# Kernel optimization log

Measured on AMD Instinct MI355X. Metric: run time of the kernel, lower is better.

Reference implementation:

```python
import math
import jax, jax.numpy as jnp
import numpy as np

D_MODEL = 1024
NUM_HEADS = 16
D_K = D_MODEL // NUM_HEADS
RANK = 16
B, L = 2, 2048


def setup_inputs() -> dict:
    key = jax.random.key(0)
    ks = jax.random.split(key, 10)
    w_scale = 0.02  # keep activations well-scaled like trained linears
    return {
        "x_q": jax.random.normal(ks[0], (B, L, D_MODEL), jnp.float32),
        "x_kv": jax.random.normal(ks[1], (B, L, D_MODEL), jnp.float32),
        "Wq": jax.random.normal(ks[2], (D_MODEL, D_MODEL), jnp.float32) * w_scale,
        "bq": jnp.zeros((D_MODEL,), jnp.float32),
        "Wk": jax.random.normal(ks[3], (D_MODEL, D_MODEL), jnp.float32) * w_scale,
        "bk": jnp.zeros((D_MODEL,), jnp.float32),
        "Wv": jax.random.normal(ks[4], (D_MODEL, D_MODEL), jnp.float32) * w_scale,
        "bv": jnp.zeros((D_MODEL,), jnp.float32),
        "Wo": jax.random.normal(ks[5], (D_MODEL, D_MODEL), jnp.float32) * w_scale,
        "bo": jnp.zeros((D_MODEL,), jnp.float32),
        "U_bil": jax.random.normal(ks[6], (NUM_HEADS, D_K, RANK), jnp.float32) * 0.02,
        "V_bil": jax.random.normal(ks[7], (NUM_HEADS, D_K, RANK), jnp.float32) * 0.02,
        "padding_mask": jnp.zeros((B, L), bool),  # True = padded KV position
    }


def reference(x_q, x_kv, Wq, bq, Wk, bk, Wv, bv, Wo, bo, U_bil, V_bil, padding_mask):
    b, l, _ = x_q.shape
    # torch nn.Linear: y = x @ W.T + b
    Q = (x_q @ Wq.T + bq).reshape(b, l, NUM_HEADS, D_K).transpose(0, 2, 1, 3)  # [B,H,L,dk]
    K = (x_kv @ Wk.T + bk).reshape(b, l, NUM_HEADS, D_K).transpose(0, 2, 1, 3)
    V = (x_kv @ Wv.T + bv).reshape(b, l, NUM_HEADS, D_K).transpose(0, 2, 1, 3)
    # low-rank bilinear projections: [B,H,L,rank]
    Q_proj = jnp.einsum("bhld,hdr->bhlr", Q, U_bil)
    K_proj = jnp.einsum("bhld,hdr->bhlr", K, V_bil)
    scores = jnp.einsum("bhqr,bhkr->bhqk", Q_proj, K_proj) / math.sqrt(RANK)  # [B,H,L,L]
    scores = jnp.where(padding_mask[:, None, None, :], jnp.float32(-10000.0), scores)
    attn = jax.nn.softmax(scores, axis=-1)  # dropout is identity in eval mode
    ctx = jnp.einsum("bhqk,bhkd->bhqd", attn, V)
    ctx = ctx.transpose(0, 2, 1, 3).reshape(b, l, D_MODEL)
    return ctx @ Wo.T + bo
```

## Files before the change

### kernel.cpp

```cpp
#include <hip/hip_runtime.h>
#include <hip/hip_bf16.h>

#define DM   1024
#define NH   16
#define DK   64
#define RK   16
#define BB   2
#define LL   2048
#define TT   (BB*LL)
#define HRK  256


typedef float f4   __attribute__((ext_vector_type(4)));
typedef float f16v __attribute__((ext_vector_type(16)));
typedef short s8v  __attribute__((ext_vector_type(8)));

static __device__ __forceinline__ unsigned short f2b(float f) {
  __hip_bfloat16 h = __float2bfloat16(f);
  unsigned short u;
  __builtin_memcpy(&u, &h, 2);
  return u;
}
static __device__ __forceinline__ float b2f(unsigned short u) {
  __hip_bfloat16 h;
  __builtin_memcpy(&h, &u, 2);
  return __bfloat162float(h);
}

__global__ __launch_bounds__(256) void cast_all(
    const float* __restrict__ s0, unsigned short* __restrict__ d0, int n0,
    const float* __restrict__ s1, unsigned short* __restrict__ d1, int n1,
    const float* __restrict__ s2, unsigned short* __restrict__ d2, int n2,
    const float* __restrict__ s3, unsigned short* __restrict__ d3, int n3) {
  const float* s; unsigned short* d; int n;
  switch (blockIdx.y) {
    case 0:  s = s0; d = d0; n = n0; break;
    case 1:  s = s1; d = d1; n = n1; break;
    case 2:  s = s2; d = d2; n = n2; break;
    default: s = s3; d = d3; n = n3; break;
  }
  for (int i = blockIdx.x*256 + threadIdx.x; i < n; i += gridDim.x*256) {
    const float4 v = ((const float4*)s)[i];
    ushort4 o;
    o.x = f2b(v.x); o.y = f2b(v.y); o.z = f2b(v.z); o.w = f2b(v.w);
    ((ushort4*)d)[i] = o;
  }
}

__global__ __launch_bounds__(256) void fuse_w(
    const float* __restrict__ Wq, const float* __restrict__ Wk,
    const float* __restrict__ Uq, const float* __restrict__ Uk,
    unsigned short* __restrict__ Aq, unsigned short* __restrict__ Ak) {
  const float* W = blockIdx.z ? Wk : Wq;
  const float* U = blockIdx.z ? Uk : Uq;
  unsigned short* At = blockIdx.z ? Ak : Aq;
  __shared__ float Us[64][16];
  __shared__ float Ws[4][64];
  const int i0 = blockIdx.x * 64;
  const int h  = blockIdx.y;
  const int tid = threadIdx.x;
  const int il = tid & 63, rr = tid >> 6;
  for (int t = tid; t < 64*16; t += 256)
    Us[t >> 4][t & 15] = U[(size_t)(h*DK + (t >> 4))*RK + (t & 15)];
  float acc[4] = {};
  for (int d0 = 0; d0 < DK; d0 += 4) {
    __syncthreads();
    Ws[rr][il] = W[(size_t)(h*DK + d0 + rr)*DM + i0 + il];
    __syncthreads();
#pragma unroll
    for (int dd = 0; dd < 4; ++dd) {
      const float w = Ws[dd][il];
#pragma unroll
      for (int j = 0; j < 4; ++j)
        acc[j] += w * Us[d0 + dd][rr*4 + j];
    }
  }
#pragma unroll
  for (int j = 0; j < 4; ++j)
    At[(size_t)(h*RK + rr*4 + j)*DM + i0 + il] = f2b(acc[j]);
}

__global__ void bias2(const float* __restrict__ bq, const float* __restrict__ bk,
                      const float* __restrict__ Uq, const float* __restrict__ Uk,
                      float* __restrict__ bpq, float* __restrict__ bpk) {
  const int t = threadIdx.x;
  const float* b = (t < 256) ? bq : bk;
  const float* U = (t < 256) ? Uq : Uk;
  float* bp = (t < 256) ? bpq : bpk;
  const int hr = t & 255, h = hr >> 4, r = hr & 15;
  float acc = 0.f;
  for (int d = 0; d < DK; ++d)
    acc += b[h*DK + d] * U[(size_t)(h*DK + d)*RK + r];
  bp[hr] = acc;
}

__global__ __launch_bounds__(256) void vsum_k(
    const unsigned short* __restrict__ Vt, float* __restrict__ Vsum) {
  const int h = blockIdx.x, b = blockIdx.y;
  const int d = threadIdx.x >> 2, part = threadIdx.x & 3;
  const unsigned short* row = Vt + ((size_t)b*DM + h*DK + d)*LL + part*512;
  float s = 0.f;
  for (int i = 0; i < 512; i += 8) {
    const s8v v = *(const s8v*)&row[i];
#pragma unroll
    for (int j = 0; j < 8; ++j) s += b2f((unsigned short)v[j]);
  }
  s += __shfl_xor(s, 1);
  s += __shfl_xor(s, 2);
  if (part == 0) Vsum[((size_t)b*NH + h)*DK + d] = s;
}

template<int N_, int MODE, int AF32>
__global__ __launch_bounds__(256) void gemm64(
    const void* __restrict__ A0, const void* __restrict__ A1,
    const unsigned short* __restrict__ B0, const unsigned short* __restrict__ B1,
    const float* __restrict__ bi0, const float* __restrict__ bi1,
    void* __restrict__ C0, void* __restrict__ C1) {
  const void* Agv = blockIdx.z ? A1 : A0;
  const unsigned short* Bg = blockIdx.z ? B1 : B0;
  const float* bias = blockIdx.z ? bi1 : bi0;
  void* Cgv = blockIdx.z ? C1 : C0;
  __shared__ unsigned short Xs[64*40];
  __shared__ unsigned short Bs[128*40];
  const int t0 = blockIdx.x * 64, n0 = blockIdx.y * 128;
  const int tid = threadIdx.x, wave = tid >> 6, lane = tid & 63;
  const int quad = lane >> 4, l15 = lane & 15;
  const int nh = wave * 32;

  const f4 z = {0.f, 0.f, 0.f, 0.f};
  f4 acc[4][2];
#pragma unroll
  for (int a = 0; a < 4; ++a) { acc[a][0] = z; acc[a][1] = z; }

  for (int k0 = 0; k0 < DM; k0 += 32) {
    __syncthreads();
    {
      const int ar = tid >> 2, ap = tid & 3;
      if (AF32) {
        const float* Af = (const float*)Agv;
        const float4 x0 = *(const float4*)&Af[(size_t)(t0 + ar)*DM + k0 + ap*8];
        const float4 x1 = *(const float4*)&Af[(size_t)(t0 + ar)*DM + k0 + ap*8 + 4];
        s8v v;
        v[0]=(short)f2b(x0.x); v[1]=(short)f2b(x0.y);
        v[2]=(short)f2b(x0.z); v[3]=(short)f2b(x0.w);
        v[4]=(short)f2b(x1.x); v[5]=(short)f2b(x1.y);
        v[6]=(short)f2b(x1.z); v[7]=(short)f2b(x1.w);
        *(s8v*)&Xs[ar*40 + ap*8] = v;
      } else {
        *(s8v*)&Xs[ar*40 + ap*8] =
            *(const s8v*)&((const unsigned short*)Agv)[(size_t)(t0 + ar)*DM + k0 + ap*8];
      }
      const int br = tid >> 1, bp = tid & 1;
      *(s8v*)&Bs[br*40 + bp*16] =
          *(const s8v*)&Bg[(size_t)(n0 + br)*DM + k0 + bp*16];
      *(s8v*)&Bs[br*40 + bp*16 + 8] =
          *(const s8v*)&Bg[(size_t)(n0 + br)*DM + k0 + bp*16 + 8];
    }
    __syncthreads();

    s8v af[4], bf[2];
#pragma unroll
    for (int ms = 0; ms < 4; ++ms)
      af[ms] = *(const s8v*)&Xs[(ms*16 + l15)*40 + quad*8];
#pragma unroll
    for (int ns = 0; ns < 2; ++ns)
      bf[ns] = *(const s8v*)&Bs[(nh + ns*16 + l15)*40 + quad*8];
#pragma unroll
    for (int ms = 0; ms < 4; ++ms)
#pragma unroll
      for (int ns = 0; ns < 2; ++ns)
        acc[ms][ns] = __builtin_amdgcn_mfma_f32_16x16x32_bf16(
            af[ms], bf[ns], acc[ms][ns], 0, 0, 0);
  }

#pragma unroll
  for (int ms = 0; ms < 4; ++ms) {
    const int tb = t0 + ms*16 + quad*4;
#pragma unroll
    for (int ns = 0; ns < 2; ++ns) {
      const int o = n0 + nh + ns*16 + l15;
      const float bv = bias[o];
      f4 a = acc[ms][ns];
      if (MODE == 0) {
        float* C = (float*)Cgv;
#pragma unroll
        for (int rg = 0; rg < 4; ++rg)
          C[(size_t)(tb + rg)*N_ + o] = a[rg] + bv;
      } else if (MODE == 1) {
        unsigned short* C = (unsigned short*)Cgv;
#pragma unroll
        for (int rg = 0; rg < 4; ++rg)
          C[(size_t)(tb + rg)*N_ + o] = f2b(a[rg] + bv);
      } else {
        unsigned short* C = (unsigned short*)Cgv;
        const int bb = tb >> 11, l = tb & 2047;
        ushort4 pk;
        pk.x = f2b(a[0] + bv); pk.y = f2b(a[1] + bv);
        pk.z = f2b(a[2] + bv); pk.w = f2b(a[3] + bv);
        *(ushort4*)&C[((size_t)bb*DM + o)*LL + l] = pk;
      }
    }
  }
}

__global__ __launch_bounds__(256) void attention_v4(
    const unsigned short* __restrict__ Qp, const unsigned short* __restrict__ Kp,
    const unsigned short* __restrict__ Vt, const float* __restrict__ Vsum,
    const unsigned char* __restrict__ msk, float* __restrict__ ctx) {
  __shared__ unsigned short Ks[64*24];
  __shared__ unsigned short Vs[64*72];
  __shared__ unsigned short Es[4][32*48];
  __shared__ float denW[4][32];
  const int q0 = blockIdx.x * 128, h = blockIdx.y, b = blockIdx.z;
  const int tid = threadIdx.x, w = tid >> 6, lane = tid & 63;
  const int l31 = lane & 31, hi = lane >> 5;
  unsigned short* __restrict__ Ew = Es[w];

  const s8v qfrag = *(const s8v*)&Qp[
      (size_t)(b*LL + q0 + w*32 + l31)*HRK + h*RK + hi*8];

  f16v acc0, acc1, z16;
#pragma unroll
  for (int i = 0; i < 16; ++i) { acc0[i] = 0.f; acc1[i] = 0.f; z16[i] = 0.f; }
  float den = 0.f;

  for (int k0 = 0; k0 < LL; k0 += 64) {
    __syncthreads();
    if (tid < 128) {
      const int row = tid >> 1, part = tid & 1;
      *(s8v*)&Ks[row*24 + part*8] =
          *(const s8v*)&Kp[(size_t)(b*LL + k0 + row)*HRK + h*RK + part*8];
    }
    {
      const int d = tid >> 2, p = tid & 3;
      const size_t gv = ((size_t)b*DM + h*DK + d)*LL + k0 + p*16;
      *(s8v*)&Vs[d*72 + p*16]     = *(const s8v*)&Vt[gv];
      *(s8v*)&Vs[d*72 + p*16 + 8] = *(const s8v*)&Vt[gv + 8];
    }
    const unsigned long long mb =
        __ballot(msk[(size_t)b*LL + k0 + lane] != 0);
    __syncthreads();

#pragma unroll
    for (int nt = 0; nt < 2; ++nt) {
      const s8v kf = *(const s8v*)&Ks[(nt*32 + l31)*24 + hi*8];
      f16v s = __builtin_amdgcn_mfma_f32_32x32x16_bf16(kf, qfrag, z16, 0, 0, 0);
#pragma unroll
      for (int r = 0; r < 4; ++r) {
        ushort4 pk;
#pragma unroll
        for (int j = 0; j < 4; ++j) {
          const int kloc = nt*32 + j + 8*r + 4*hi;
          float em = __expf(s[r*4 + j] * 0.25f);
          if ((mb >> kloc) & 1ull) em = 0.f;
          den += em;
          ((unsigned short*)&pk)[j] = f2b(em - 1.f);
        }
        *(ushort4*)&Ew[l31*48 + nt*32 + r*8 + 4*hi] = pk;
      }
    }
#pragma unroll
    for (int kc = 0; kc < 4; ++kc) {
      const s8v ef  = *(const s8v*)&Ew[l31*48 + kc*16 + hi*8];
      const s8v vf0 = *(const s8v*)&Vs[l31*72 + kc*16 + hi*8];
      const s8v vf1 = *(const s8v*)&Vs[(32 + l31)*72 + kc*16 + hi*8];
      acc0 = __builtin_amdgcn_mfma_f32_32x32x16_bf16(ef, vf0, acc0, 0, 0, 0);
      acc1 = __builtin_amdgcn_mfma_f32_32x32x16_bf16(ef, vf1, acc1, 0, 0, 0);
    }
  }

  den += __shfl_xor(den, 32);
  if (hi == 0) denW[w][l31] = 1.f / fmaxf(den, 1e-30f);

  const float vs0 = Vsum[((size_t)b*NH + h)*DK + l31];
  const float vs1 = Vsum[((size_t)b*NH + h)*DK + 32 + l31];

#pragma unroll
  for (int rg = 0; rg < 16; ++rg) {
    const int qr = (rg & 3) + 8*(rg >> 2) + 4*hi;
    const float inv = denW[w][qr];
    const size_t row = (size_t)(b*LL + q0 + w*32 + qr)*DM + h*DK;
    ctx[row + l31]      = (vs0 + acc0[rg]) * inv;
    ctx[row + 32 + l31] = (vs1 + acc1[rg]) * inv;
  }
}

extern "C" void kernel_launch(void* const* d_in, const int* in_sizes, int n_in,
                              void* d_out, int out_size, void* d_ws, size_t ws_size,
                              hipStream_t stream) {
  (void)in_sizes; (void)n_in; (void)out_size; (void)ws_size;
  const float* x_q   = (const float*)d_in[0];
  const float* x_kv  = (const float*)d_in[1];
  const float* Wq    = (const float*)d_in[2];
  const float* bq    = (const float*)d_in[3];
  const float* Wk    = (const float*)d_in[4];
  const float* bk    = (const float*)d_in[5];
  const float* Wv    = (const float*)d_in[6];
  const float* bv    = (const float*)d_in[7];
  const float* Wo    = (const float*)d_in[8];
  const float* bo    = (const float*)d_in[9];
  const float* U_bil = (const float*)d_in[10];
  const float* V_bil = (const float*)d_in[11];
  const unsigned char* pmask = (const unsigned char*)d_in[12];
  float* out = (float*)d_out;

  char* w = (char*)d_ws;
  unsigned short* xq_b  = (unsigned short*)(w);
  unsigned short* xkv_b = (unsigned short*)(w +  8388608);
  unsigned short* Wv_b  = (unsigned short*)(w + 16777216);
  unsigned short* Wo_b  = (unsigned short*)(w + 18874368);
  unsigned short* Atq   = (unsigned short*)(w + 20971520);
  unsigned short* Atk   = (unsigned short*)(w + 21495808);
  float*          bpq   = (float*)(w + 22020096);
  float*          bpk   = (float*)(w + 22021120);
  unsigned short* Qp    = (unsigned short*)(w + 22022144);
  unsigned short* Kp    = (unsigned short*)(w + 24119296);
  unsigned short* Vt    = (unsigned short*)(w + 26216448);
  float*          Vsum  = (float*)(w + 34605056);
  float*          ctx   = (float*)w;

  cast_all<<<dim3(1024, 4), 256, 0, stream>>>(
      x_q, xq_b, TT*DM/4, x_kv, xkv_b, TT*DM/4,
      Wv, Wv_b, DM*DM/4,  Wo, Wo_b, DM*DM/4);
  fuse_w<<<dim3(DM/64, NH, 2), 256, 0, stream>>>(Wq, Wk, U_bil, V_bil, Atq, Atk);
  bias2<<<1, 512, 0, stream>>>(bq, bk, U_bil, V_bil, bpq, bpk);
  gemm64<HRK, 1, 0><<<dim3(64, 2, 2), 256, 0, stream>>>(
      xq_b, xkv_b, Atq, Atk, bpq, bpk, Qp, Kp);
  gemm64<DM, 2, 0><<<dim3(64, 8, 1), 256, 0, stream>>>(
      xkv_b, xkv_b, Wv_b, Wv_b, bv, bv, Vt, Vt);
  vsum_k<<<dim3(NH, BB), 256, 0, stream>>>(Vt, Vsum);
  attention_v4<<<dim3(LL/128, NH, BB), 256, 0, stream>>>(
      Qp, Kp, Vt, Vsum, pmask, ctx);
  gemm64<DM, 0, 1><<<dim3(64, 8, 1), 256, 0, stream>>>(
      ctx, ctx, Wo_b, Wo_b, bo, bo, out, out);
}
```

Baseline: 274.6 us.

## Double-buffer K/V tiles with register prefetch and keep softmax probabilities in registers

Rewrites the attention kernel to double-buffer the K and V tiles in shared memory, prefetching the next tile into registers so global loads overlap compute. One barrier per iteration replaces two. Probabilities are packed with v_cvt_pk_bf16_f32 and rearranged into MFMA operand layout with cross-half lane shuffles instead of a round trip through shared memory. A fast path also skips per-element masking when a tile has no padded keys. These changes add register pressure and shuffle work in exchange for less LDS traffic and fewer synchronisations.

New measurement: 276.7 us. Within noise of the previous version (+0.8%).

```diff
diff --git a/kernel.cpp b/kernel.cpp
--- a/kernel.cpp
+++ b/kernel.cpp
@@ -14,6 +14,8 @@
 typedef float f4   __attribute__((ext_vector_type(4)));
 typedef float f16v __attribute__((ext_vector_type(16)));
 typedef short s8v  __attribute__((ext_vector_type(8)));
+typedef unsigned int u2v __attribute__((ext_vector_type(2)));
+typedef unsigned int u4v __attribute__((ext_vector_type(4)));
 
 static __device__ __forceinline__ unsigned short f2b(float f) {
   __hip_bfloat16 h = __float2bfloat16(f);
@@ -203,70 +205,127 @@
   }
 }
 
-__global__ __launch_bounds__(256) void attention_v4(
+template<bool MASKED>
+static __device__ __forceinline__ void softmax_pack(
+    const f16v& s0, const f16v& s1, const unsigned long long mb, const int hi,
+    float& den, unsigned int (&Pd)[2][4][2]) {
+#pragma unroll
+  for (int nt = 0; nt < 2; ++nt) {
+    const f16v& sv = nt ? s1 : s0;
+#pragma unroll
+    for (int r = 0; r < 4; ++r) {
+      float ep[4];
+#pragma unroll
+      for (int j = 0; j < 4; ++j) {
+        float em = __expf(sv[r*4 + j] * 0.25f);
+        if (MASKED) {
+          const int kloc = nt*32 + j + 8*r + 4*hi;
+          if ((mb >> kloc) & 1ull) em = 0.f;
+        }
+        den += em;
+        ep[j] = em - 1.f;
+      }
+      asm("v_cvt_pk_bf16_f32 %0, %1, %2"
+          : "=v"(Pd[nt][r][0]) : "v"(ep[0]), "v"(ep[1]));
+      asm("v_cvt_pk_bf16_f32 %0, %1, %2"
+          : "=v"(Pd[nt][r][1]) : "v"(ep[2]), "v"(ep[3]));
+    }
+  }
+}
+
+__global__ __launch_bounds__(256) void attention_v5(
     const unsigned short* __restrict__ Qp, const unsigned short* __restrict__ Kp,
     const unsigned short* __restrict__ Vt, const float* __restrict__ Vsum,
     const unsigned char* __restrict__ msk, float* __restrict__ ctx) {
-  __shared__ unsigned short Ks[64*24];
-  __shared__ unsigned short Vs[64*72];
-  __shared__ unsigned short Es[4][32*48];
+  __shared__ __align__(16) unsigned short Ks[2][2][64][8];
+  __shared__ __align__(16) unsigned short Vs[2][8][64][8];
   __shared__ float denW[4][32];
   const int q0 = blockIdx.x * 128, h = blockIdx.y, b = blockIdx.z;
   const int tid = threadIdx.x, w = tid >> 6, lane = tid & 63;
   const int l31 = lane & 31, hi = lane >> 5;
-  unsigned short* __restrict__ Ew = Es[w];
 
   const s8v qfrag = *(const s8v*)&Qp[
       (size_t)(b*LL + q0 + w*32 + l31)*HRK + h*RK + hi*8];
 
+  const int sr = tid >> 2, sp = tid & 3;
+  const unsigned short* __restrict__ Vrow =
+      Vt + ((size_t)b*DM + h*DK + sr)*LL;
+  const unsigned short* __restrict__ Kbase =
+      Kp + ((size_t)b*LL + sr)*HRK + h*RK + sp*4;
+  const unsigned char*  __restrict__ Mrow = msk + (size_t)b*LL + lane;
+
+  u2v kpre; s8v vpre0, vpre1;
+  unsigned char mcur, mnext;
+
+  kpre  = *(const u2v*)&Kbase[0];
+  vpre0 = *(const s8v*)&Vrow[sp*16];
+  vpre1 = *(const s8v*)&Vrow[sp*16 + 8];
+  mcur  = Mrow[0];
+  *(u2v*)&Ks[0][sp>>1][sr][(sp&1)*4] = kpre;
+  *(s8v*)&Vs[0][sp*2][sr][0]   = vpre0;
+  *(s8v*)&Vs[0][sp*2+1][sr][0] = vpre1;
+  kpre  = *(const u2v*)&Kbase[(size_t)64*HRK];
+  vpre0 = *(const s8v*)&Vrow[64 + sp*16];
+  vpre1 = *(const s8v*)&Vrow[64 + sp*16 + 8];
+  mnext = Mrow[64];
+  __syncthreads();
+
   f16v acc0, acc1, z16;
 #pragma unroll
   for (int i = 0; i < 16; ++i) { acc0[i] = 0.f; acc1[i] = 0.f; z16[i] = 0.f; }
   float den = 0.f;
 
-  for (int k0 = 0; k0 < LL; k0 += 64) {
-    __syncthreads();
-    if (tid < 128) {
-      const int row = tid >> 1, part = tid & 1;
-      *(s8v*)&Ks[row*24 + part*8] =
-          *(const s8v*)&Kp[(size_t)(b*LL + k0 + row)*HRK + h*RK + part*8];
-    }
-    {
-      const int d = tid >> 2, p = tid & 3;
-      const size_t gv = ((size_t)b*DM + h*DK + d)*LL + k0 + p*16;
-      *(s8v*)&Vs[d*72 + p*16]     = *(const s8v*)&Vt[gv];
-      *(s8v*)&Vs[d*72 + p*16 + 8] = *(const s8v*)&Vt[gv + 8];
-    }
-    const unsigned long long mb =
-        __ballot(msk[(size_t)b*LL + k0 + lane] != 0);
-    __syncthreads();
-
-#pragma unroll
-    for (int nt = 0; nt < 2; ++nt) {
-      const s8v kf = *(const s8v*)&Ks[(nt*32 + l31)*24 + hi*8];
-      f16v s = __builtin_amdgcn_mfma_f32_32x32x16_bf16(kf, qfrag, z16, 0, 0, 0);
-#pragma unroll
-      for (int r = 0; r < 4; ++r) {
-        ushort4 pk;
-#pragma unroll
-        for (int j = 0; j < 4; ++j) {
-          const int kloc = nt*32 + j + 8*r + 4*hi;
-          float em = __expf(s[r*4 + j] * 0.25f);
-          if ((mb >> kloc) & 1ull) em = 0.f;
-          den += em;
-          ((unsigned short*)&pk)[j] = f2b(em - 1.f);
-        }
-        *(ushort4*)&Ew[l31*48 + nt*32 + r*8 + 4*hi] = pk;
-      }
-    }
+  for (int t = 0; t < LL/64; ++t) {
+    const int cur = t & 1;
+    const unsigned long long mb = __ballot(mcur != 0);
+
+    const s8v kf0 = *(const s8v*)&Ks[cur][hi][l31][0];
+    const s8v kf1 = *(const s8v*)&Ks[cur][hi][32 + l31][0];
+    s8v vf[4][2];
 #pragma unroll
     for (int kc = 0; kc < 4; ++kc) {
-      const s8v ef  = *(const s8v*)&Ew[l31*48 + kc*16 + hi*8];
-      const s8v vf0 = *(const s8v*)&Vs[l31*72 + kc*16 + hi*8];
-      const s8v vf1 = *(const s8v*)&Vs[(32 + l31)*72 + kc*16 + hi*8];
-      acc0 = __builtin_amdgcn_mfma_f32_32x32x16_bf16(ef, vf0, acc0, 0, 0, 0);
-      acc1 = __builtin_amdgcn_mfma_f32_32x32x16_bf16(ef, vf1, acc1, 0, 0, 0);
-    }
+      vf[kc][0] = *(const s8v*)&Vs[cur][kc*2 + hi][l31][0];
+      vf[kc][1] = *(const s8v*)&Vs[cur][kc*2 + hi][32 + l31][0];
+    }
+
+    const f16v s0 = __builtin_amdgcn_mfma_f32_32x32x16_bf16(kf0, qfrag, z16, 0, 0, 0);
+    const f16v s1 = __builtin_amdgcn_mfma_f32_32x32x16_bf16(kf1, qfrag, z16, 0, 0, 0);
+
+    unsigned int Pd[2][4][2];
+    if (__builtin_expect(mb != 0ull, 0))
+      softmax_pack<true >(s0, s1, mb, hi, den, Pd);
+    else
+      softmax_pack<false>(s0, s1, mb, hi, den, Pd);
+
+#pragma unroll
+    for (int kc = 0; kc < 4; ++kc) {
+      const int nt = kc >> 1, a = (kc & 1)*2;
+      const unsigned int p00 = Pd[nt][a][0],   p01 = Pd[nt][a][1];
+      const unsigned int p10 = Pd[nt][a+1][0], p11 = Pd[nt][a+1][1];
+      const unsigned int e0 = __shfl_xor(hi ? p00 : p10, 32);
+      const unsigned int e1 = __shfl_xor(hi ? p01 : p11, 32);
+      u4v efi;
+      efi[0] = hi ? e0 : p00;
+      efi[1] = hi ? e1 : p01;
+      efi[2] = hi ? p10 : e0;
+      efi[3] = hi ? p11 : e1;
+      const s8v ef = __builtin_bit_cast(s8v, efi);
+      acc0 = __builtin_amdgcn_mfma_f32_32x32x16_bf16(ef, vf[kc][0], acc0, 0, 0, 0);
+      acc1 = __builtin_amdgcn_mfma_f32_32x32x16_bf16(ef, vf[kc][1], acc1, 0, 0, 0);
+    }
+
+    if (t + 1 < LL/64) {
+      *(u2v*)&Ks[cur^1][sp>>1][sr][(sp&1)*4] = kpre;
+      *(s8v*)&Vs[cur^1][sp*2][sr][0]   = vpre0;
+      *(s8v*)&Vs[cur^1][sp*2+1][sr][0] = vpre1;
+      const int tn = (t + 2 < LL/64) ? t + 2 : LL/64 - 1;
+      kpre  = *(const u2v*)&Kbase[(size_t)tn*64*HRK];
+      vpre0 = *(const s8v*)&Vrow[tn*64 + sp*16];
+      vpre1 = *(const s8v*)&Vrow[tn*64 + sp*16 + 8];
+      mcur  = mnext;
+      mnext = Mrow[tn*64];
+    }
+    __syncthreads();
   }
 
   den += __shfl_xor(den, 32);
@@ -329,7 +388,7 @@
   gemm64<DM, 2, 0><<<dim3(64, 8, 1), 256, 0, stream>>>(
       xkv_b, xkv_b, Wv_b, Wv_b, bv, bv, Vt, Vt);
   vsum_k<<<dim3(NH, BB), 256, 0, stream>>>(Vt, Vsum);
-  attention_v4<<<dim3(LL/128, NH, BB), 256, 0, stream>>>(
+  attention_v5<<<dim3(LL/128, NH, BB), 256, 0, stream>>>(
       Qp, Kp, Vt, Vsum, pmask, ctx);
   gemm64<DM, 0, 1><<<dim3(64, 8, 1), 256, 0, stream>>>(
       ctx, ctx, Wo_b, Wo_b, bo, bo, out, out);
```
